# Optimization experiments

Measured on AMD Instinct MI355X. Metric: run time of the kernel, lower is better.

The kernel has to match this reference:

```python
import jax, jax.numpy as jnp
import numpy as np

B, Q, K, D, H, DH = 4, 512, 4096, 1024, 8, 128  # qk_channels=v_channels=out=1024

def setup_inputs() -> dict:
    key = jax.random.key(0)
    ks = jax.random.split(key, 5)
    s = 1.0 / np.sqrt(D)
    return {
        "inputs_q": jax.random.normal(ks[0], (B, Q, D), jnp.float32),
        "inputs_kv": jax.random.normal(ks[1], (B, K, D), jnp.float32),
        "Wq": jax.random.normal(ks[2], (D, H, DH), jnp.float32) * s,
        "Wkv": jax.random.normal(ks[3], (D, H, 2 * DH), jnp.float32) * s,
        "Wproj": jax.random.normal(ks[4], (H, DH, D), jnp.float32) * (1.0 / np.sqrt(H * DH)),
        "b_proj": jnp.zeros((D,), jnp.float32),
    }

def reference(inputs_q, inputs_kv, Wq, Wkv, Wproj, b_proj):
    # QKV projections (no bias)
    q = jnp.einsum('bqd,dhe->bqhe', inputs_q, Wq)          # [B,Q,H,DH]
    kv = jnp.einsum('bkd,dhe->bkhe', inputs_kv, Wkv)        # [B,K,H,2*DH]
    k, v = kv[..., :DH], kv[..., DH:]
    # scaled dot-product attention (softmax in fp32, per source)
    attn = jnp.einsum('bqhd,bkhd->bhqk', q, k) / np.sqrt(DH)
    attn = jax.nn.softmax(attn.astype(jnp.float32), axis=-1).astype(v.dtype)
    o = jnp.einsum('bhqk,bkhd->bqhd', attn, v)              # [B,Q,H,DH]
    # output projection contracting (head, head_dim), with bias
    return jnp.einsum('bqhd,hdo->bqo', o, Wproj) + b_proj   # [B,Q,D]
```

## Files before the change

### kernel.cpp

```cpp
#include <hip/hip_runtime.h>
#include <hip/hip_bf16.h>
#include <cstdint>

typedef unsigned short u16;
typedef unsigned int u32;
typedef __bf16 bf16x8 __attribute__((ext_vector_type(8)));
typedef u16 u16x8 __attribute__((ext_vector_type(8)));
typedef u16 u16x4 __attribute__((ext_vector_type(4)));
typedef float f32x4 __attribute__((ext_vector_type(4)));

#define MFMA16(a, b, c) __builtin_amdgcn_mfma_f32_16x16x32_bf16(a, b, c, 0, 0, 0)

__device__ __forceinline__ void async16(const void* g, void* s) {
    __builtin_amdgcn_global_load_lds((const __attribute__((address_space(1))) void*)g,
                                     (__attribute__((address_space(3))) void*)s, 16, 0, 0);
}

__device__ __forceinline__ u16 f2bf(float f) {
    u32 u; __builtin_memcpy(&u, &f, 4);
    u = u + 0x7fffu + ((u >> 16) & 1u);
    return (u16)(u >> 16);
}

__global__ __launch_bounds__(256) void convert_inputs(const float* __restrict__ inq,
                                                      u16* __restrict__ Aq,
                                                      const float* __restrict__ inkv,
                                                      u16* __restrict__ Akv) {
    const int blk = blockIdx.x;
    const float* in; u16* out; size_t i;
    if (blk < 1024) { in = inq;  out = Aq;  i = (size_t)blk * 256 + threadIdx.x; }
    else            { in = inkv; out = Akv; i = (size_t)(blk - 1024) * 256 + threadIdx.x; }
    const float4* p = (const float4*)in + i * 2;
    const float4 a = p[0], b = p[1];
    u16x8 v;
    v[0] = f2bf(a.x); v[1] = f2bf(a.y); v[2] = f2bf(a.z); v[3] = f2bf(a.w);
    v[4] = f2bf(b.x); v[5] = f2bf(b.y); v[6] = f2bf(b.z); v[7] = f2bf(b.w);
    ((u16x8*)out)[i] = v;
}

__global__ __launch_bounds__(256) void prep_weights(const float* __restrict__ Wq,  u16* __restrict__ WqT,
                                                    const float* __restrict__ Wkv, u16* __restrict__ WkvT,
                                                    const float* __restrict__ Wp,  u16* __restrict__ WpT) {
    __shared__ u16 t[64][65];
    const int blk = blockIdx.x;
    const float* in; u16* out; int R, C, bx, by;
    if (blk < 256)      { in = Wq;  out = WqT;  R = 1024; C = 1024; bx = blk & 15;  by = blk >> 4; }
    else if (blk < 768) { in = Wkv; out = WkvT; R = 1024; C = 2048; bx = (blk - 256) & 31; by = (blk - 256) >> 5; }
    else                { in = Wp;  out = WpT;  R = 1024; C = 1024; bx = (blk - 768) & 15; by = (blk - 768) >> 4; }
    const int r0 = by << 6, c0 = bx << 6;
    const int tid = threadIdx.x;
#pragma unroll
    for (int i = 0; i < 16; i++) {
        int idx = i * 256 + tid;
        int r = idx >> 6, c = idx & 63;
        t[r][c] = f2bf(in[(size_t)(r0 + r) * C + c0 + c]);
    }
    __syncthreads();
#pragma unroll
    for (int i = 0; i < 16; i++) {
        int idx = i * 256 + tid;
        int c = idx >> 6, r = idx & 63;
        out[(size_t)(c0 + c) * R + r0 + r] = t[r][c];
    }
}

template <bool OUTF32, int NT, bool VFUSE>
__global__ __launch_bounds__(256) void gemm_bt(const u16* __restrict__ A,
                                               const u16* __restrict__ B,
                                               void* __restrict__ Cv,
                                               const float* __restrict__ bias,
                                               u16* __restrict__ Vt,
                                               int M, int N, int K) {
    constexpr int NJ = NT / 32;
    __shared__ __align__(16) u16 As[128 * 64];
    __shared__ __align__(16) u16 Bs[NT * 64];
    const int tid = threadIdx.x;
    const int wave = tid >> 6, lane = tid & 63;
    const int lrow = lane & 15, quad = lane >> 4;
    const int nb = N / NT;
    const int bx = blockIdx.x % nb, by = blockIdx.x / nb;
    const long m0 = (long)by << 7, n0 = (long)bx * NT;
    const int wm = (wave >> 1) << 6, wn = (wave & 1) * (NT / 2);

    const f32x4 fz = {0.f, 0.f, 0.f, 0.f};
    f32x4 acc[4][NJ];
#pragma unroll
    for (int i = 0; i < 4; i++)
#pragma unroll
        for (int j = 0; j < NJ; j++) acc[i][j] = fz;

    const int srow = wave * 8 + (lane >> 3);
    const int scol = ((lane & 7) ^ (lane >> 3)) << 3;
    const u16* Ag = A + (m0 + srow) * K + scol;
    const u16* Bg = B + (n0 + srow) * K + scol;
    u16* AsW = &As[wave * 512];
    u16* BsW = &Bs[wave * 512];

    for (int k0 = 0; k0 < K; k0 += 64) {
        __syncthreads();
#pragma unroll
        for (int c = 0; c < 4; c++)
            async16(Ag + (long)c * 32 * K + k0, AsW + c * 2048);
#pragma unroll
        for (int c = 0; c < NT / 32; c++)
            async16(Bg + (long)c * 32 * K + k0, BsW + c * 2048);
        __syncthreads();
#pragma unroll
        for (int c = 0; c < 2; c++) {
            bf16x8 af[4], bfr[NJ];
#pragma unroll
            for (int i = 0; i < 4; i++) {
                const int row = wm + i * 16 + lrow;
                af[i] = *(const bf16x8*)&As[row * 64 + (((c * 4 + quad) ^ (row & 7)) << 3)];
            }
#pragma unroll
            for (int j = 0; j < NJ; j++) {
                const int row = wn + j * 16 + lrow;
                bfr[j] = *(const bf16x8*)&Bs[row * 64 + (((c * 4 + quad) ^ (row & 7)) << 3)];
            }
#pragma unroll
            for (int i = 0; i < 4; i++)
#pragma unroll
                for (int j = 0; j < NJ; j++)
                    acc[i][j] = MFMA16(af[i], bfr[j], acc[i][j]);
        }
    }
    if (VFUSE && (bx & 1)) {
#pragma unroll
        for (int j = 0; j < NJ; j++) {
            const int col = (int)n0 + wn + j * 16 + lrow;
            const int h = col >> 8, dh = (col & 255) - 128;
#pragma unroll
            for (int i = 0; i < 4; i++) {
                const int row = (int)m0 + wm + i * 16 + quad * 4;
                const int b = row >> 12, kv = row & 4095;
                u16x4 pk;
#pragma unroll
                for (int r = 0; r < 4; r++) pk[r] = f2bf(acc[i][j][r]);
                *(u16x4*)&Vt[(((size_t)b * 8 + h) * 128 + dh) * 4096 + kv] = pk;
            }
        }
        return;
    }
#pragma unroll
    for (int j = 0; j < NJ; j++) {
        const long col = n0 + wn + j * 16 + lrow;
        const float bv = bias ? bias[col] : 0.0f;
#pragma unroll
        for (int i = 0; i < 4; i++) {
            const long row = m0 + wm + i * 16 + quad * 4;
#pragma unroll
            for (int r = 0; r < 4; r++) {
                const float v = acc[i][j][r] + bv;
                if (OUTF32) ((float*)Cv)[(row + r) * N + col] = v;
                else        ((u16*)Cv)[(row + r) * N + col] = f2bf(v);
            }
        }
    }
}

__global__ __launch_bounds__(512) void flash_attn_split(const u16* __restrict__ qb,
                                                        const u16* __restrict__ kvb,
                                                        const u16* __restrict__ vTb,
                                                        float* __restrict__ Opart,
                                                        float* __restrict__ Mpart,
                                                        float* __restrict__ Lpart) {
    __shared__ __align__(16) u16 Ks[64 * 128];
    __shared__ __align__(16) u16 Vs[128 * 64];
    __shared__ __align__(16) u16 Ps[8][16 * 64];
    const int tid = threadIdx.x, wave = tid >> 6, lane = tid & 63;
    const int lrow = lane & 15, quad = lane >> 4;
    const int blk = blockIdx.x;
    const int split = blk & 3, qt = (blk >> 2) & 3, h = (blk >> 4) & 7, b = blk >> 7;
    const int q0 = qt * 128;
    const int kbase = split * 1024;

    bf16x8 qf[4];
    {
        const u16* qp = qb + (((size_t)(b * 512 + q0 + wave * 16 + lrow) * 8 + h) << 7) + quad * 8;
#pragma unroll
        for (int c = 0; c < 4; c++) qf[c] = *(const bf16x8*)(qp + c * 32);
    }

    const f32x4 fz = {0.f, 0.f, 0.f, 0.f};
    f32x4 oacc[8];
#pragma unroll
    for (int g = 0; g < 8; g++) oacc[g] = fz;
    float mrow = -1e30f, lsum = 0.f;
    const float scale = 0.08838834764831845f;

    const int kRow = tid >> 4, kBlk = tid & 15;
    const int vRow = tid >> 3, vBlk = tid & 7;
    const u16* kg = kvb + (size_t)b * 4096 * 2048 + h * 256 + kBlk * 8;
    const u16* vg = vTb + (size_t)(b * 8 + h) * 128 * 4096 + vBlk * 8;

    for (int k0 = kbase; k0 < kbase + 1024; k0 += 64) {
        __syncthreads();
#pragma unroll
        for (int i = 0; i < 2; i++) {
            const int r = i * 32 + kRow;
            *(bf16x8*)&Ks[r * 128 + ((kBlk ^ (r & 15)) << 3)] =
                *(const bf16x8*)&kg[(size_t)(k0 + r) * 2048];
            const int rv = i * 64 + vRow;
            *(bf16x8*)&Vs[rv * 64 + ((vBlk ^ (rv & 7)) << 3)] =
                *(const bf16x8*)&vg[(size_t)rv * 4096 + k0];
        }
        __syncthreads();

        f32x4 s[4];
#pragma unroll
        for (int t = 0; t < 4; t++) {
            f32x4 a = fz;
#pragma unroll
            for (int c = 0; c < 4; c++) {
                const bf16x8 kf = *(const bf16x8*)
                    &Ks[(t * 16 + lrow) * 128 + (((c * 4 + quad) ^ lrow) << 3)];
                a = MFMA16(kf, qf[c], a);
            }
            s[t] = a * scale;
        }

        float mx = s[0][0];
#pragma unroll
        for (int t = 0; t < 4; t++)
#pragma unroll
            for (int r = 0; r < 4; r++) mx = fmaxf(mx, s[t][r]);
        mx = fmaxf(mx, __shfl_xor(mx, 16));
        mx = fmaxf(mx, __shfl_xor(mx, 32));
        const float mn = fmaxf(mrow, mx);
        const float alpha = __expf(mrow - mn);
        mrow = mn;
        float sum = 0.f;
#pragma unroll
        for (int t = 0; t < 4; t++)
#pragma unroll
            for (int r = 0; r < 4; r++) {
                float p = __expf(s[t][r] - mn);
                s[t][r] = p;
                sum += p;
            }
        sum += __shfl_xor(sum, 16);
        sum += __shfl_xor(sum, 32);
        lsum = lsum * alpha + sum;

        u16* Pw = &Ps[wave][0];
#pragma unroll
        for (int t = 0; t < 4; t++) {
            u16x4 pk;
#pragma unroll
            for (int r = 0; r < 4; r++) pk[r] = f2bf(s[t][r]);
            const int kvo = t * 16 + quad * 4;
            *(u16x4*)&Pw[lrow * 64 + (((kvo >> 3) ^ (lrow & 7)) << 3) + (kvo & 7)] = pk;
        }
        asm volatile("s_waitcnt lgkmcnt(0)" ::: "memory");
        const bf16x8 pf0 = *(const bf16x8*)&Pw[lrow * 64 + ((quad ^ (lrow & 7)) << 3)];
        const bf16x8 pf1 = *(const bf16x8*)&Pw[lrow * 64 + (((4 + quad) ^ (lrow & 7)) << 3)];

#pragma unroll
        for (int g = 0; g < 8; g++) {
            f32x4 o = oacc[g] * alpha;
            o = MFMA16(*(const bf16x8*)&Vs[(g * 16 + lrow) * 64 + ((quad ^ (lrow & 7)) << 3)], pf0, o);
            o = MFMA16(*(const bf16x8*)&Vs[(g * 16 + lrow) * 64 + (((4 + quad) ^ (lrow & 7)) << 3)], pf1, o);
            oacc[g] = o;
        }
    }

    float* Ob = Opart + (size_t)blk * 16384;
#pragma unroll
    for (int g = 0; g < 8; g++)
        *(f32x4*)&Ob[(wave * 16 + lrow) * 128 + g * 16 + quad * 4] = oacc[g];
    if (quad == 0) {
        const int row = blk * 128 + wave * 16 + lrow;
        Mpart[row] = mrow;
        Lpart[row] = lsum;
    }
}

__global__ __launch_bounds__(512) void combine_attn(const float* __restrict__ Opart,
                                                    const float* __restrict__ Mpart,
                                                    const float* __restrict__ Lpart,
                                                    u16* __restrict__ ob) {
    const int c = blockIdx.x;
    const int qt = c & 3, h = (c >> 2) & 7, b = c >> 5;
    const int lr = threadIdx.x >> 2, cg = (threadIdx.x & 3) * 32;
    float ms[4], w[4];
    float m = -1e30f;
#pragma unroll
    for (int s = 0; s < 4; s++) { ms[s] = Mpart[(c * 4 + s) * 128 + lr]; m = fmaxf(m, ms[s]); }
    float l = 0.f;
#pragma unroll
    for (int s = 0; s < 4; s++) { w[s] = __expf(ms[s] - m); l += w[s] * Lpart[(c * 4 + s) * 128 + lr]; }
    const float inv = 1.f / l;
#pragma unroll
    for (int s = 0; s < 4; s++) w[s] *= inv;
    const size_t orow = ((size_t)(b * 512 + qt * 128 + lr) * 8 + h) << 7;
#pragma unroll
    for (int j = 0; j < 4; j++) {
        f32x4 a0 = {0.f, 0.f, 0.f, 0.f}, a1 = a0;
#pragma unroll
        for (int s = 0; s < 4; s++) {
            const f32x4* p = (const f32x4*)(Opart + ((size_t)(c * 4 + s)) * 16384 + (size_t)lr * 128 + cg + j * 8);
            a0 += p[0] * w[s];
            a1 += p[1] * w[s];
        }
        u16x8 v;
#pragma unroll
        for (int i = 0; i < 4; i++) { v[i] = f2bf(a0[i]); v[4 + i] = f2bf(a1[i]); }
        *(u16x8*)&ob[orow + cg + j * 8] = v;
    }
}

extern "C" void kernel_launch(void* const* d_in, const int* in_sizes, int n_in,
                              void* d_out, int out_size, void* d_ws, size_t ws_size,
                              hipStream_t stream) {
    const float* inq   = (const float*)d_in[0];
    const float* inkv  = (const float*)d_in[1];
    const float* Wq    = (const float*)d_in[2];
    const float* Wkv   = (const float*)d_in[3];
    const float* Wproj = (const float*)d_in[4];
    const float* bproj = (const float*)d_in[5];
    float* out = (float*)d_out;

    u16* WqT    = (u16*)d_ws;
    u16* WkvT   = WqT + (size_t)1024 * 1024;
    u16* WprojT = WkvT + (size_t)2048 * 1024;
    u16* Aq     = WprojT + (size_t)1024 * 1024;
    u16* Akv    = Aq + (size_t)2048 * 1024;
    u16* qbuf   = Akv + (size_t)16384 * 1024;
    u16* kvbuf  = qbuf + (size_t)2048 * 1024;
    u16* vTbuf  = kvbuf + (size_t)16384 * 2048;
    u16* obuf   = vTbuf + (size_t)32 * 128 * 4096;

    float* Opart = (float*)Akv;
    float* Mpart = (float*)Aq;
    float* Lpart = Mpart + 65536;

    convert_inputs<<<9216, 256, 0, stream>>>(inq, Aq, inkv, Akv);
    prep_weights<<<1024, 256, 0, stream>>>(Wq, WqT, Wkv, WkvT, Wproj, WprojT);

    gemm_bt<false, 64, false><<<16 * 16, 256, 0, stream>>>(Aq, WqT, qbuf, nullptr, nullptr, 2048, 1024, 1024);
    gemm_bt<false, 128, true><<<128 * 16, 256, 0, stream>>>(Akv, WkvT, kvbuf, nullptr, vTbuf, 16384, 2048, 1024);

    flash_attn_split<<<512, 512, 0, stream>>>(qbuf, kvbuf, vTbuf, Opart, Mpart, Lpart);
    combine_attn<<<128, 512, 0, stream>>>(Opart, Mpart, Lpart, obuf);

    gemm_bt<true, 64, false><<<16 * 16, 256, 0, stream>>>(obuf, WprojT, (void*)out, bproj, nullptr, 2048, 1024, 1024);
}
```

Before: 326.0 us.

## Replace KV projection GEMM with 256x256 double-buffered pipelined kernel

Adds a dedicated KV projection kernel that uses 256x256 tiles, 512 threads, double-buffered async global-to-LDS loads interleaved with MFMA phases under setprio, and a grid swizzle for L2 locality. Each tile covers one head, so the K half is written normally and the V half is written transposed for the attention kernel. The goal is higher MFMA utilisation and overlap of loads with compute on the largest GEMM. The cost is heavy register and LDS use and hand-tuned waitcnt logic that could be fragile.

```diff
diff --git a/kernel.cpp b/kernel.cpp
--- a/kernel.cpp
+++ b/kernel.cpp
@@ -64,12 +64,11 @@
     }
 }
 
-template <bool OUTF32, int NT, bool VFUSE>
+template <bool OUTF32, int NT>
 __global__ __launch_bounds__(256) void gemm_bt(const u16* __restrict__ A,
                                                const u16* __restrict__ B,
                                                void* __restrict__ Cv,
                                                const float* __restrict__ bias,
-                                               u16* __restrict__ Vt,
                                                int M, int N, int K) {
     constexpr int NJ = NT / 32;
     __shared__ __align__(16) u16 As[128 * 64];
@@ -125,23 +124,6 @@
                     acc[i][j] = MFMA16(af[i], bfr[j], acc[i][j]);
         }
     }
-    if (VFUSE && (bx & 1)) {
-#pragma unroll
-        for (int j = 0; j < NJ; j++) {
-            const int col = (int)n0 + wn + j * 16 + lrow;
-            const int h = col >> 8, dh = (col & 255) - 128;
-#pragma unroll
-            for (int i = 0; i < 4; i++) {
-                const int row = (int)m0 + wm + i * 16 + quad * 4;
-                const int b = row >> 12, kv = row & 4095;
-                u16x4 pk;
-#pragma unroll
-                for (int r = 0; r < 4; r++) pk[r] = f2bf(acc[i][j][r]);
-                *(u16x4*)&Vt[(((size_t)b * 8 + h) * 128 + dh) * 4096 + kv] = pk;
-            }
-        }
-        return;
-    }
 #pragma unroll
     for (int j = 0; j < NJ; j++) {
         const long col = n0 + wn + j * 16 + lrow;
@@ -154,6 +136,159 @@
                 const float v = acc[i][j][r] + bv;
                 if (OUTF32) ((float*)Cv)[(row + r) * N + col] = v;
                 else        ((u16*)Cv)[(row + r) * N + col] = f2bf(v);
+            }
+        }
+    }
+}
+
+__global__ __launch_bounds__(512, 2) void gemm_kv256(const u16* __restrict__ A,
+                                                     const u16* __restrict__ B,
+                                                     u16* __restrict__ C,
+                                                     u16* __restrict__ Vt) {
+    constexpr int K = 1024, N = 2048, NT = 16;
+    __shared__ __align__(16) u16 As[2][256 * 64];
+    __shared__ __align__(16) u16 Bs[2][256 * 64];
+    const int tid = threadIdx.x;
+    const int wave = tid >> 6, lane = tid & 63;
+    const int lrow = lane & 15, quad = lane >> 4;
+    const int wMi = wave >> 2, wNi = wave & 3;
+    const int wm = wMi * 128, wn = wNi * 64;
+    const int wg = blockIdx.x;
+    const int swz = (wg & 7) * 64 + (wg >> 3);
+    const int bx = swz & 7, by = swz >> 3;
+    const long m0 = (long)by << 8, n0 = (long)bx << 8;
+
+    const int srow = tid >> 3;
+    const int scol = ((tid & 7) ^ (srow & 7)) << 3;
+    const u16* Ag = A + (m0 + srow) * K + scol;
+    const u16* Bg = B + (n0 + srow) * K + scol;
+    const int sdst = tid * 8;
+
+    auto stgA = [&](int bi, int h, int kt) {
+        async16(Ag + (size_t)(h * 128) * K + kt * 64,      &As[bi][h * 8192 + sdst]);
+        async16(Ag + (size_t)(h * 128 + 64) * K + kt * 64, &As[bi][h * 8192 + 4096 + sdst]);
+    };
+    auto stgB = [&](int bi, int h, int kt) {
+        async16(Bg + (size_t)(h * 128) * K + kt * 64,      &Bs[bi][h * 8192 + sdst]);
+        async16(Bg + (size_t)(h * 128 + 64) * K + kt * 64, &Bs[bi][h * 8192 + 4096 + sdst]);
+    };
+
+    stgB(0, 0, 0); stgB(0, 1, 0); stgA(0, 0, 0); stgA(0, 1, 0);
+    stgB(1, 0, 1); stgB(1, 1, 1); stgA(1, 0, 1);
+
+    const f32x4 fz = {0.f, 0.f, 0.f, 0.f};
+    f32x4 acc[8][4];
+#pragma unroll
+    for (int i = 0; i < 8; i++)
+#pragma unroll
+        for (int j = 0; j < 4; j++) acc[i][j] = fz;
+
+    asm volatile("s_waitcnt vmcnt(6)" ::: "memory");
+    __builtin_amdgcn_s_barrier();
+
+    bf16x8 av[4][2], bv[4][2];
+    for (int t = 0; t < NT; ++t) {
+        const int cur = t & 1, nxt = cur ^ 1;
+#pragma unroll
+        for (int i = 0; i < 4; i++) {
+            const int row = wm + i * 16 + lrow;
+#pragma unroll
+            for (int c = 0; c < 2; c++)
+                av[i][c] = *(const bf16x8*)&As[cur][row * 64 + (((c * 4 + quad) ^ (row & 7)) << 3)];
+        }
+#pragma unroll
+        for (int j = 0; j < 4; j++) {
+            const int row = wn + j * 16 + lrow;
+#pragma unroll
+            for (int c = 0; c < 2; c++)
+                bv[j][c] = *(const bf16x8*)&Bs[cur][row * 64 + (((c * 4 + quad) ^ (row & 7)) << 3)];
+        }
+        if (t + 1 < NT) stgA(nxt, 1, t + 1);
+        __builtin_amdgcn_s_barrier();
+        asm volatile("s_waitcnt lgkmcnt(0)" ::: "memory");
+        __builtin_amdgcn_s_setprio(1);
+#pragma unroll
+        for (int i = 0; i < 4; i++)
+#pragma unroll
+            for (int j = 0; j < 2; j++)
+#pragma unroll
+                for (int c = 0; c < 2; c++)
+                    acc[i][j] = MFMA16(av[i][c], bv[j][c], acc[i][j]);
+        __builtin_amdgcn_s_setprio(0);
+        __builtin_amdgcn_s_barrier();
+        if (t + 2 < NT) stgB(cur, 0, t + 2);
+        __builtin_amdgcn_s_barrier();
+        __builtin_amdgcn_s_setprio(1);
+#pragma unroll
+        for (int i = 0; i < 4; i++)
+#pragma unroll
+            for (int j = 2; j < 4; j++)
+#pragma unroll
+                for (int c = 0; c < 2; c++)
+                    acc[i][j] = MFMA16(av[i][c], bv[j][c], acc[i][j]);
+        __builtin_amdgcn_s_setprio(0);
+        __builtin_amdgcn_s_barrier();
+#pragma unroll
+        for (int i = 0; i < 4; i++) {
+            const int row = wm + (i + 4) * 16 + lrow;
+#pragma unroll
+            for (int c = 0; c < 2; c++)
+                av[i][c] = *(const bf16x8*)&As[cur][row * 64 + (((c * 4 + quad) ^ (row & 7)) << 3)];
+        }
+        if (t + 2 < NT) stgB(cur, 1, t + 2);
+        __builtin_amdgcn_s_barrier();
+        asm volatile("s_waitcnt lgkmcnt(0)" ::: "memory");
+        __builtin_amdgcn_s_setprio(1);
+#pragma unroll
+        for (int i = 0; i < 4; i++)
+#pragma unroll
+            for (int j = 0; j < 2; j++)
+#pragma unroll
+                for (int c = 0; c < 2; c++)
+                    acc[i + 4][j] = MFMA16(av[i][c], bv[j][c], acc[i + 4][j]);
+        __builtin_amdgcn_s_setprio(0);
+        __builtin_amdgcn_s_barrier();
+        if (t + 2 < NT) stgA(cur, 0, t + 2);
+        __builtin_amdgcn_s_barrier();
+        __builtin_amdgcn_s_setprio(1);
+#pragma unroll
+        for (int i = 0; i < 4; i++)
+#pragma unroll
+            for (int j = 2; j < 4; j++)
+#pragma unroll
+                for (int c = 0; c < 2; c++)
+                    acc[i + 4][j] = MFMA16(av[i][c], bv[j][c], acc[i + 4][j]);
+        __builtin_amdgcn_s_setprio(0);
+        if (t + 2 < NT)      { asm volatile("s_waitcnt vmcnt(6)" ::: "memory"); }
+        else if (t + 1 < NT) { asm volatile("s_waitcnt vmcnt(0)" ::: "memory"); }
+        __builtin_amdgcn_s_barrier();
+    }
+
+    const int h = bx;
+    if (wNi < 2) {
+#pragma unroll
+        for (int j = 0; j < 4; j++) {
+            const long col = n0 + wn + j * 16 + lrow;
+#pragma unroll
+            for (int i = 0; i < 8; i++) {
+                const long row = m0 + wm + i * 16 + quad * 4;
+#pragma unroll
+                for (int r = 0; r < 4; r++)
+                    C[(row + r) * N + col] = f2bf(acc[i][j][r]);
+            }
+        }
+    } else {
+#pragma unroll
+        for (int j = 0; j < 4; j++) {
+            const int dh = (wNi - 2) * 64 + j * 16 + lrow;
+#pragma unroll
+            for (int i = 0; i < 8; i++) {
+                const int row = (int)m0 + wm + i * 16 + quad * 4;
+                const int b = row >> 12, kv = row & 4095;
+                u16x4 pk;
+#pragma unroll
+                for (int r = 0; r < 4; r++) pk[r] = f2bf(acc[i][j][r]);
+                *(u16x4*)&Vt[(((size_t)b * 8 + h) * 128 + dh) * 4096 + kv] = pk;
             }
         }
     }
@@ -338,11 +473,11 @@
     convert_inputs<<<9216, 256, 0, stream>>>(inq, Aq, inkv, Akv);
     prep_weights<<<1024, 256, 0, stream>>>(Wq, WqT, Wkv, WkvT, Wproj, WprojT);
 
-    gemm_bt<false, 64, false><<<16 * 16, 256, 0, stream>>>(Aq, WqT, qbuf, nullptr, nullptr, 2048, 1024, 1024);
-    gemm_bt<false, 128, true><<<128 * 16, 256, 0, stream>>>(Akv, WkvT, kvbuf, nullptr, vTbuf, 16384, 2048, 1024);
+    gemm_bt<false, 64><<<16 * 16, 256, 0, stream>>>(Aq, WqT, qbuf, nullptr, 2048, 1024, 1024);
+    gemm_kv256<<<512, 512, 0, stream>>>(Akv, WkvT, kvbuf, vTbuf);
 
     flash_attn_split<<<512, 512, 0, stream>>>(qbuf, kvbuf, vTbuf, Opart, Mpart, Lpart);
     combine_attn<<<128, 512, 0, stream>>>(Opart, Mpart, Lpart, obuf);
 
-    gemm_bt<true, 64, false><<<16 * 16, 256, 0, stream>>>(obuf, WprojT, (void*)out, bproj, nullptr, 2048, 1024, 1024);
-}
+    gemm_bt<true, 64><<<16 * 16, 256, 0, stream>>>(obuf, WprojT, (void*)out, bproj, 2048, 1024, 1024);
+}
```

Measured after the change: 305.1 us. 1.07x faster.
